# Kernel optimization log

Hardware: AMD Instinct MI355X
Metric: run time of the kernel (lower is better)

The kernel has to match this reference:

```python
import jax, jax.numpy as jnp
import numpy as np

N = 4096  # nmentions
# Static index sets: strict lower triangle in row-major order (matches torch
# boolean-mask assignment order) and the diagonal.
ROWS, COLS = np.tril_indices(N, -1)
DIAG = np.arange(N)


def setup_inputs() -> dict:
    key = jax.random.key(0)
    k1, k2, k3 = jax.random.split(key, 3)
    eps_scores = jax.random.normal(k1, (N,), dtype=jnp.float32)
    ana_scores = jax.random.normal(k2, (N * (N - 1) // 2,), dtype=jnp.float32)
    # Build a coherent solution mask: random cluster ids; a mention's correct
    # antecedents are earlier mentions of the same cluster, else itself (epsilon).
    clusters = np.asarray(jax.random.randint(k3, (N,), 0, N // 8))
    same = clusters[:, None] == clusters[None, :]
    lower = np.tril(np.ones((N, N), dtype=bool), -1)
    sol_link = same & lower
    has_ante = sol_link.any(axis=1)
    mask = sol_link.astype(np.float32)
    mask[DIAG, DIAG] = (~has_ante).astype(np.float32)
    link_costs = jnp.array([[0.5], [1.0]], dtype=jnp.float32)  # [false_link],[wrong_link]
    false_new_cost = jnp.array([1.5], dtype=jnp.float32)
    return {
        "eps_scores": eps_scores,
        "ana_scores": ana_scores,
        "solution_mask": jnp.asarray(mask),
        "link_costs": link_costs,
        "false_new_cost": false_new_cost,
    }


def create_score_matrix(eps_scores, ana_scores):
    # [N,N]: diagonal = epsilon (non-anaphoric) scores, strict lower triangle =
    # pairwise antecedent scores in row-major tril order; upper triangle zero.
    scores = jnp.zeros((N, N), dtype=eps_scores.dtype)
    scores = scores.at[DIAG, DIAG].set(eps_scores)
    scores = scores.at[ROWS, COLS].set(ana_scores)
    return scores


def reference(eps_scores, ana_scores, solution_mask, link_costs, false_new_cost):
    scores = create_score_matrix(eps_scores, ana_scores)
    minimum_score = scores.min()
    solution_scores = solution_mask * scores + (1.0 - solution_mask) * minimum_score
    best_correct = solution_scores.max(axis=1)  # [N]
    non_anaphoric = jnp.diagonal(solution_mask)  # [N]
    # anaphoricity_selector @ link_costs.expand(2, N): each row is a constant
    # equal to false_link if non-anaphoric else wrong_link.
    row_cost = non_anaphoric * link_costs[0, 0] + (1.0 - non_anaphoric) * link_costs[1, 0]
    potential_costs = jnp.tril(jnp.broadcast_to(row_cost[:, None], (N, N)), -1)
    potential_costs = potential_costs.at[DIAG, DIAG].set(false_new_cost[0])
    cost_matrix = (1.0 - solution_mask) * potential_costs
    loss_values = cost_matrix * (1.0 + scores - best_correct[:, None])
    loss_per_example = loss_values.max(axis=1)  # [N]
    return loss_per_example
```

## Files before the change

kernel.cpp:

```cpp
#include <hip/hip_runtime.h>

#define N 4096
#define BLK 256

typedef float f4u __attribute__((ext_vector_type(4), aligned(4)));
typedef float f4a __attribute__((ext_vector_type(4), aligned(16)));

__global__ __launch_bounds__(BLK) void mention_loss_kernel(
    const float* __restrict__ eps_scores,
    const float* __restrict__ ana_scores,
    const float* __restrict__ mask,
    const float* __restrict__ link_costs,
    const float* __restrict__ false_new_cost,
    float* __restrict__ out)
{
    const int row = N - 1 - (int)blockIdx.x;
    const int tid = threadIdx.x;
    const long long base = (long long)row * (row - 1) / 2;
    const float* __restrict__ mrow = mask + (size_t)row * (size_t)N;

    float bc  = -3.4e38f;
    float sm0 = -3.4e38f;

    int p = (int)((4 - (base & 3)) & 3);
    if (p > row) p = row;
    const int nvec = (row - p) >> 2;
    const int t0   = p + (nvec << 2);

#pragma unroll 4
    for (int g = tid; g < nvec; g += BLK) {
        const int j = p + (g << 2);
        const f4a s4 = *(const f4a*)(ana_scores + base + j);
        const f4u m4 = *(const f4u*)(mrow + j);
        #pragma unroll
        for (int k = 0; k < 4; ++k) {
            const float s = s4[k], m = m4[k];
            if (m != 0.0f) bc  = fmaxf(bc,  s);
            else           sm0 = fmaxf(sm0, s);
        }
    }
    if (tid < p) {
        const float s = ana_scores[base + tid], m = mrow[tid];
        if (m != 0.0f) bc = fmaxf(bc, s); else sm0 = fmaxf(sm0, s);
    }
    if (tid < row - t0) {
        const int j = t0 + tid;
        const float s = ana_scores[base + j], m = mrow[j];
        if (m != 0.0f) bc = fmaxf(bc, s); else sm0 = fmaxf(sm0, s);
    }

    for (int off = 32; off; off >>= 1) {
        bc  = fmaxf(bc,  __shfl_down(bc,  off));
        sm0 = fmaxf(sm0, __shfl_down(sm0, off));
    }
    __shared__ float r_bc[BLK / 64], r_sm[BLK / 64];
    if ((tid & 63) == 0) { r_bc[tid >> 6] = bc; r_sm[tid >> 6] = sm0; }
    __syncthreads();
    if (tid == 0) {
        float B = r_bc[0], S = r_sm[0];
        for (int w = 1; w < BLK / 64; ++w) {
            B = fmaxf(B, r_bc[w]);
            S = fmaxf(S, r_sm[w]);
        }
        const float e = eps_scores[row];
        const float d = mrow[row];
        if (d != 0.0f) B = fmaxf(B, e);
        const float rc = d * link_costs[0] + (1.0f - d) * link_costs[1];
        float loss = fmaxf(0.0f, rc * (1.0f + S - B));
        if (d == 0.0f) loss = fmaxf(loss, false_new_cost[0] * (1.0f + e - B));
        out[row] = loss;
    }
}

extern "C" void kernel_launch(void* const* d_in, const int* in_sizes, int n_in,
                              void* d_out, int out_size, void* d_ws, size_t ws_size,
                              hipStream_t stream) {
    const float* eps  = (const float*)d_in[0];
    const float* ana  = (const float*)d_in[1];
    const float* mask = (const float*)d_in[2];
    const float* lc   = (const float*)d_in[3];
    const float* fnc  = (const float*)d_in[4];
    float* out = (float*)d_out;

    mention_loss_kernel<<<N, BLK, 0, stream>>>(eps, ana, mask, lc, fnc, out);
}
```

Before: 119.0 us.

## Pair long and short triangular rows per block and use nontemporal loads

Each block now processes two rows, row N-1-b and row b, so that every block does roughly equal work over the triangular score layout, and the grid is halved. The scan uses four independent branchless max accumulators instead of branching, plus nontemporal loads for the streamed score and mask data. This targets load imbalance and tail effects from the varying row lengths. In exchange each block has less memory-level parallelism and there are half as many blocks to spread across CUs.

New measurement: 124.4 us. +4.6%, slower.

```diff
diff --git a/kernel.cpp b/kernel.cpp
--- a/kernel.cpp
+++ b/kernel.cpp
@@ -2,9 +2,70 @@
 
 #define N 4096
 #define BLK 256
+#define NEGF (-3.4e38f)
 
 typedef float f4u __attribute__((ext_vector_type(4), aligned(4)));
 typedef float f4a __attribute__((ext_vector_type(4), aligned(16)));
+
+__device__ __forceinline__ void scan_row(
+    const float* __restrict__ ana_scores,
+    const float* __restrict__ mask,
+    const int row, const int tid,
+    float& bc_out, float& sm_out)
+{
+    const long long base = (long long)row * (row - 1) / 2;
+    const float* __restrict__ arow = ana_scores + base;
+    const float* __restrict__ mrow = mask + (size_t)row * (size_t)N;
+
+    float bc0 = NEGF, bc1 = NEGF, bc2 = NEGF, bc3 = NEGF;
+    float sm0 = NEGF, sm1 = NEGF, sm2 = NEGF, sm3 = NEGF;
+
+    int p = (int)((4 - (base & 3)) & 3);
+    if (p > row) p = row;
+    const int nvec = (row - p) >> 2;
+    const int t0   = p + (nvec << 2);
+
+#pragma unroll 4
+    for (int g = tid; g < nvec; g += BLK) {
+        const int j = p + (g << 2);
+        const f4a s4 = __builtin_nontemporal_load((const f4a*)(arow + j));
+        const f4u m4 = __builtin_nontemporal_load((const f4u*)(mrow + j));
+        const bool o0 = (m4[0] != 0.0f);
+        const bool o1 = (m4[1] != 0.0f);
+        const bool o2 = (m4[2] != 0.0f);
+        const bool o3 = (m4[3] != 0.0f);
+        bc0 = fmaxf(bc0, o0 ? s4[0] : NEGF);
+        sm0 = fmaxf(sm0, o0 ? NEGF : s4[0]);
+        bc1 = fmaxf(bc1, o1 ? s4[1] : NEGF);
+        sm1 = fmaxf(sm1, o1 ? NEGF : s4[1]);
+        bc2 = fmaxf(bc2, o2 ? s4[2] : NEGF);
+        sm2 = fmaxf(sm2, o2 ? NEGF : s4[2]);
+        bc3 = fmaxf(bc3, o3 ? s4[3] : NEGF);
+        sm3 = fmaxf(sm3, o3 ? NEGF : s4[3]);
+    }
+    if (tid < p) {
+        const float s = arow[tid], m = mrow[tid];
+        if (m != 0.0f) bc0 = fmaxf(bc0, s); else sm0 = fmaxf(sm0, s);
+    }
+    if (tid < row - t0) {
+        const int j = t0 + tid;
+        const float s = arow[j], m = mrow[j];
+        if (m != 0.0f) bc1 = fmaxf(bc1, s); else sm1 = fmaxf(sm1, s);
+    }
+    bc_out = fmaxf(fmaxf(bc0, bc1), fmaxf(bc2, bc3));
+    sm_out = fmaxf(fmaxf(sm0, sm1), fmaxf(sm2, sm3));
+}
+
+__device__ __forceinline__ float row_loss(
+    float B, float S, const float e, const float d,
+    const float lc0, const float lc1, const float fn)
+{
+    if (d != 0.0f) B = fmaxf(B, e);
+    const float rc = d * lc0 + (1.0f - d) * lc1;
+    float loss = fmaxf(0.0f, rc * (1.0f + S - B));
+    if (d == 0.0f) loss = fmaxf(loss, fn * (1.0f + e - B));
+    return loss;
+}
 
 __global__ __launch_bounds__(BLK) void mention_loss_kernel(
     const float* __restrict__ eps_scores,
@@ -14,61 +75,42 @@
     const float* __restrict__ false_new_cost,
     float* __restrict__ out)
 {
-    const int row = N - 1 - (int)blockIdx.x;
-    const int tid = threadIdx.x;
-    const long long base = (long long)row * (row - 1) / 2;
-    const float* __restrict__ mrow = mask + (size_t)row * (size_t)N;
+    const int b    = (int)blockIdx.x;
+    const int rowA = N - 1 - b;
+    const int rowB = b;
+    const int tid  = threadIdx.x;
 
-    float bc  = -3.4e38f;
-    float sm0 = -3.4e38f;
-
-    int p = (int)((4 - (base & 3)) & 3);
-    if (p > row) p = row;
-    const int nvec = (row - p) >> 2;
-    const int t0   = p + (nvec << 2);
-
-#pragma unroll 4
-    for (int g = tid; g < nvec; g += BLK) {
-        const int j = p + (g << 2);
-        const f4a s4 = *(const f4a*)(ana_scores + base + j);
-        const f4u m4 = *(const f4u*)(mrow + j);
-        #pragma unroll
-        for (int k = 0; k < 4; ++k) {
-            const float s = s4[k], m = m4[k];
-            if (m != 0.0f) bc  = fmaxf(bc,  s);
-            else           sm0 = fmaxf(sm0, s);
-        }
-    }
-    if (tid < p) {
-        const float s = ana_scores[base + tid], m = mrow[tid];
-        if (m != 0.0f) bc = fmaxf(bc, s); else sm0 = fmaxf(sm0, s);
-    }
-    if (tid < row - t0) {
-        const int j = t0 + tid;
-        const float s = ana_scores[base + j], m = mrow[j];
-        if (m != 0.0f) bc = fmaxf(bc, s); else sm0 = fmaxf(sm0, s);
-    }
+    float bcA, smA, bcB, smB;
+    scan_row(ana_scores, mask, rowA, tid, bcA, smA);
+    scan_row(ana_scores, mask, rowB, tid, bcB, smB);
 
     for (int off = 32; off; off >>= 1) {
-        bc  = fmaxf(bc,  __shfl_down(bc,  off));
-        sm0 = fmaxf(sm0, __shfl_down(sm0, off));
+        bcA = fmaxf(bcA, __shfl_down(bcA, off));
+        smA = fmaxf(smA, __shfl_down(smA, off));
+        bcB = fmaxf(bcB, __shfl_down(bcB, off));
+        smB = fmaxf(smB, __shfl_down(smB, off));
     }
-    __shared__ float r_bc[BLK / 64], r_sm[BLK / 64];
-    if ((tid & 63) == 0) { r_bc[tid >> 6] = bc; r_sm[tid >> 6] = sm0; }
+    __shared__ float r[4][BLK / 64];
+    if ((tid & 63) == 0) {
+        const int w = tid >> 6;
+        r[0][w] = bcA; r[1][w] = smA; r[2][w] = bcB; r[3][w] = smB;
+    }
     __syncthreads();
     if (tid == 0) {
-        float B = r_bc[0], S = r_sm[0];
+        float BA = r[0][0], SA = r[1][0], BB = r[2][0], SB = r[3][0];
+#pragma unroll
         for (int w = 1; w < BLK / 64; ++w) {
-            B = fmaxf(B, r_bc[w]);
-            S = fmaxf(S, r_sm[w]);
+            BA = fmaxf(BA, r[0][w]); SA = fmaxf(SA, r[1][w]);
+            BB = fmaxf(BB, r[2][w]); SB = fmaxf(SB, r[3][w]);
         }
-        const float e = eps_scores[row];
-        const float d = mrow[row];
-        if (d != 0.0f) B = fmaxf(B, e);
-        const float rc = d * link_costs[0] + (1.0f - d) * link_costs[1];
-        float loss = fmaxf(0.0f, rc * (1.0f + S - B));
-        if (d == 0.0f) loss = fmaxf(loss, false_new_cost[0] * (1.0f + e - B));
-        out[row] = loss;
+        const float lc0 = link_costs[0], lc1 = link_costs[1];
+        const float fn  = false_new_cost[0];
+        const float eA = eps_scores[rowA];
+        const float dA = mask[(size_t)rowA * N + rowA];
+        const float eB = eps_scores[rowB];
+        const float dB = mask[(size_t)rowB * N + rowB];
+        out[rowA] = row_loss(BA, SA, eA, dA, lc0, lc1, fn);
+        out[rowB] = row_loss(BB, SB, eB, dB, lc0, lc1, fn);
     }
 }
 
@@ -82,5 +124,5 @@
     const float* fnc  = (const float*)d_in[4];
     float* out = (float*)d_out;
 
-    mention_loss_kernel<<<N, BLK, 0, stream>>>(eps, ana, mask, lc, fnc, out);
+    mention_loss_kernel<<<N / 2, BLK, 0, stream>>>(eps, ana, mask, lc, fnc, out);
 }
```
